# Kernel optimization log

Measured on AMD Instinct MI355X. Metric: run time of the kernel, lower is better.

Reference implementation:

```python
import jax, jax.numpy as jnp
import numpy as np

B, S, H, D, DEPTH = 2, 96, 96, 96, 8  # eval path requires S == H == D
USER_DEPTH_INDEX = 3


def setup_inputs() -> dict:
    key = jax.random.key(0)
    k1, k2, k3, k4 = jax.random.split(key, 4)
    Q = jax.random.normal(k1, (B, S, H, D), dtype=jnp.float32)
    K = jax.random.normal(k2, (B, S, H, D), dtype=jnp.float32)
    V = jax.random.normal(k3, (B, S, H, D), dtype=jnp.float32)
    # xavier_uniform for depth_weights (depth, D, D): bound = sqrt(6/(fan_in+fan_out))
    bound = float(np.sqrt(6.0 / (D + D)))
    depth_weights = jax.random.uniform(k4, (DEPTH, D, D), dtype=jnp.float32,
                                       minval=-bound, maxval=bound)
    return {"Q": Q, "K": K, "V": V, "depth_weights": depth_weights,
            "user_depth_index": USER_DEPTH_INDEX}


def reference(Q, K, V, depth_weights, user_depth_index):
    # Eval (self.training=False) path of ModifiedMistralAttention, faithful to
    # torch view/permute/squeeze semantics. Q,K,V: (B, S, H, D) with S==H==D.
    b, sq, h, d = Q.shape
    scale = jnp.asarray(1.0 / np.sqrt(d), Q.dtype)
    # torch .view -> reshape (reinterpret, NOT a transpose)
    q5 = Q.reshape(b, h, sq, d, 1)
    k5 = K.reshape(b, h, sq, 1, d)
    # matmul (D,1)@(1,D) == per-position outer product; squeeze(-1) is a no-op (D!=1)
    attn_5d = (q5 * k5) * scale                      # (B,H,S,D,D)
    attn_5d = jnp.transpose(attn_5d, (0, 1, 3, 4, 2))  # (B,H,D,D,S)

    v_re = jnp.transpose(V, (0, 2, 1, 3))            # (B,H,S,D)
    tv = jnp.einsum('bhqi,dij->bhqjd', v_re, depth_weights)  # (B,H,S,D,DEPTH)
    tv = jnp.transpose(tv, (0, 2, 1, 3, 4))          # (B,S,H,D,DEPTH)

    # hard gather by fixed depth index
    sel_v = jnp.transpose(tv[..., user_depth_index], (0, 2, 1, 3))  # (B,H,S,D)
    attn_w = jnp.swapaxes(attn_5d[..., user_depth_index], -1, -2)   # (B,H,D,D)

    out = jnp.einsum('bhqk,bkhv->bqhv', attn_w, sel_v)  # (B,D,S,D); needs S=H=D
    out = jnp.transpose(out, (0, 2, 1, 3)).reshape(b, sq, -1)  # (B,S,D*D)
    return out
```

## Files before the change

### kernel.cpp

```cpp
#include <hip/hip_runtime.h>

#define BB 2
#define SS 96
#define DD 96
#define BH (BB * SS)
#define DSQ (DD * DD)

__global__ __launch_bounds__(256) void
mistral_mod_attn_kernel(const float* __restrict__ Q,
                        const float* __restrict__ K,
                        const float* __restrict__ V,
                        const float* __restrict__ DW,
                        const int* __restrict__ udi_p,
                        float* __restrict__ out) {
    const int bh  = blockIdx.x;
    const int tid = threadIdx.x;
    const int udi = *udi_p;

    __shared__ float q_lds[DD];
    __shared__ float t_lds[DD];
    __shared__ float r_lds[DD];
    __shared__ float kq_lds[DD];

    const long base = (long)bh * DSQ;
    const float scale = 0.10206207261596575f;

    if (tid < DD) {
        q_lds[tid]  = Q[base + (long)udi * DD + tid];
        kq_lds[tid] = K[base + (long)udi * DD + tid] * scale;
    }
    __syncthreads();

    if (tid < DD) {
        float acc = 0.0f;
        const float* vp = V + base + tid;
        #pragma unroll 8
        for (int k = 0; k < DD; ++k) acc += q_lds[k] * vp[k * DD];
        t_lds[tid] = acc;
    }
    __syncthreads();

    if (tid < DD) {
        float acc = 0.0f;
        const float* wp = DW + (long)udi * DSQ + tid;
        #pragma unroll 8
        for (int i = 0; i < DD; ++i) acc += t_lds[i] * wp[i * DD];
        r_lds[tid] = acc;
    }
    __syncthreads();

    float* op = out + base;
    for (int idx = tid; idx < DSQ; idx += 256) {
        int q = idx / DD;
        int v = idx - q * DD;
        op[idx] = kq_lds[q] * r_lds[v];
    }
}

extern "C" void kernel_launch(void* const* d_in, const int* in_sizes, int n_in,
                              void* d_out, int out_size, void* d_ws, size_t ws_size,
                              hipStream_t stream) {
    const float* Q  = (const float*)d_in[0];
    const float* K  = (const float*)d_in[1];
    const float* V  = (const float*)d_in[2];
    const float* DW = (const float*)d_in[3];
    const int* udi  = (const int*)d_in[4];
    float* out = (float*)d_out;

    mistral_mod_attn_kernel<<<BH, 256, 0, stream>>>(Q, K, V, DW, udi, out);
}
```

Measured before the change: 80.04 us.

## Split matvec reductions across 4 thread groups and vectorize output stores

Raises the block to 384 threads and splits each of the two 96-long matrix-vector reductions into 4 chunks, one per thread group, combining the partial sums through shared memory. This engages all threads instead of 96, cutting the serial dependent-load chain per thread. The outer-product output write switches to float4 stores. The cost is two extra barriers and a small shared partial-sum buffer.

```diff
diff --git a/kernel.cpp b/kernel.cpp
--- a/kernel.cpp
+++ b/kernel.cpp
@@ -1,12 +1,13 @@
 #include <hip/hip_runtime.h>
 
-#define BB 2
-#define SS 96
 #define DD 96
-#define BH (BB * SS)
+#define BH 192
 #define DSQ (DD * DD)
+#define NT 384
+#define KSPLIT 4
+#define KCH (DD / KSPLIT)
 
-__global__ __launch_bounds__(256) void
+__global__ __launch_bounds__(NT) void
 mistral_mod_attn_kernel(const float* __restrict__ Q,
                         const float* __restrict__ K,
                         const float* __restrict__ V,
@@ -18,42 +19,58 @@
     const int udi = *udi_p;
 
     __shared__ float q_lds[DD];
+    __shared__ float kq_lds[DD];
+    __shared__ float part[KSPLIT][DD];
     __shared__ float t_lds[DD];
     __shared__ float r_lds[DD];
-    __shared__ float kq_lds[DD];
 
     const long base = (long)bh * DSQ;
     const float scale = 0.10206207261596575f;
 
     if (tid < DD) {
-        q_lds[tid]  = Q[base + (long)udi * DD + tid];
-        kq_lds[tid] = K[base + (long)udi * DD + tid] * scale;
+        q_lds[tid] = Q[base + (long)udi * DD + tid];
+    } else if (tid < 2 * DD) {
+        const int i = tid - DD;
+        kq_lds[i] = K[base + (long)udi * DD + i] * scale;
     }
     __syncthreads();
 
-    if (tid < DD) {
+    const int i = tid % DD;
+    const int p = tid / DD;
+
+    {
         float acc = 0.0f;
-        const float* vp = V + base + tid;
-        #pragma unroll 8
-        for (int k = 0; k < DD; ++k) acc += q_lds[k] * vp[k * DD];
-        t_lds[tid] = acc;
+        const float* vp = V + base + (long)(p * KCH) * DD + i;
+        #pragma unroll
+        for (int k = 0; k < KCH; ++k) acc += q_lds[p * KCH + k] * vp[k * DD];
+        part[p][i] = acc;
     }
     __syncthreads();
+    if (tid < DD)
+        t_lds[tid] = part[0][tid] + part[1][tid] + part[2][tid] + part[3][tid];
+    __syncthreads();
 
-    if (tid < DD) {
+    {
         float acc = 0.0f;
-        const float* wp = DW + (long)udi * DSQ + tid;
-        #pragma unroll 8
-        for (int i = 0; i < DD; ++i) acc += t_lds[i] * wp[i * DD];
-        r_lds[tid] = acc;
+        const float* wp = DW + (long)udi * DSQ + (long)(p * KCH) * DD + i;
+        #pragma unroll
+        for (int k = 0; k < KCH; ++k) acc += t_lds[p * KCH + k] * wp[k * DD];
+        part[p][i] = acc;
     }
     __syncthreads();
+    if (tid < DD)
+        r_lds[tid] = part[0][tid] + part[1][tid] + part[2][tid] + part[3][tid];
+    __syncthreads();
 
-    float* op = out + base;
-    for (int idx = tid; idx < DSQ; idx += 256) {
-        int q = idx / DD;
-        int v = idx - q * DD;
-        op[idx] = kq_lds[q] * r_lds[v];
+    float4* op4 = (float4*)(out + base);
+    for (int idx4 = tid; idx4 < DSQ / 4; idx4 += NT) {
+        const int q  = idx4 / (DD / 4);
+        const int v4 = idx4 - q * (DD / 4);
+        const float kqv = kq_lds[q];
+        const float4 rr = *(const float4*)&r_lds[v4 * 4];
+        float4 o;
+        o.x = kqv * rr.x; o.y = kqv * rr.y; o.z = kqv * rr.z; o.w = kqv * rr.w;
+        op4[idx4] = o;
     }
 }
 
@@ -67,5 +84,5 @@
     const int* udi  = (const int*)d_in[4];
     float* out = (float*)d_out;
 
-    mistral_mod_attn_kernel<<<BH, 256, 0, stream>>>(Q, K, V, DW, udi, out);
+    mistral_mod_attn_kernel<<<BH, NT, 0, stream>>>(Q, K, V, DW, udi, out);
 }
```

After: 76.18 us. -4.8%, faster.
